# Optimization experiments

Hardware: AMD Instinct MI355X
Metric: run time of the kernel (lower is better)

## Reference

```python
import jax, jax.numpy as jnp
import numpy as np


def setup_inputs() -> dict:
    key = jax.random.key(0)
    ks = jax.random.split(key, 6)
    B, N, S, D, A = 32, 12, 512, 256, 96
    return {
        "value": jax.random.normal(ks[0], (B, N, S, D), dtype=jnp.float32),
        "emb": jax.random.normal(ks[1], (N, S, A), dtype=jnp.float32),
        "Wqk": jax.random.normal(ks[2], (A, D), dtype=jnp.float32) * (A ** -0.5),
        "bqk": jax.random.normal(ks[3], (D,), dtype=jnp.float32) * 0.02,
        "Wv": jax.random.normal(ks[4], (D, D), dtype=jnp.float32) * (D ** -0.5),
        "bv": jax.random.normal(ks[5], (D,), dtype=jnp.float32) * 0.02,
    }


def reference(value, emb, Wqk, bqk, Wv, bv):
    # qk: [n, s, d] -- query and key share the same projection FC_Q_K
    qk = emb @ Wqk + bqk
    v = value @ Wv + bv                      # [b, n, s, d]
    q = jax.nn.softmax(qk, axis=-1)          # softmax over d (last dim of query)
    k = jax.nn.softmax(qk.swapaxes(-1, -2), axis=-1)  # [n, d, s], softmax over s
    # key @ value: [n, d, s] x [b, n, s, e] -> [b, n, d, e] (broadcast over b)
    kv = jnp.einsum('nds,bnse->bnde', k, v)
    # query @ kv: [n, s, d] x [b, n, d, e] -> [b, n, s, e]
    out = jnp.einsum('nsd,bnde->bnse', q, kv)
    return out
```

## Files before the change

### kernel.cpp

```cpp
#include <hip/hip_runtime.h>
#include <hip/hip_bf16.h>

#define B_ 32
#define N_ 12
#define S_ 512
#define D_ 256
#define A_ 96

typedef __attribute__((ext_vector_type(8))) short short8;
typedef __attribute__((ext_vector_type(4))) float float4v;

static __device__ __forceinline__ ushort f2bf(float f) {
  union { float f; unsigned u; } a;
  a.f = f;
  return (ushort)((a.u + 0x7FFFu + ((a.u >> 16) & 1u)) >> 16);
}

__global__ __launch_bounds__(256) void k_qk_softmax_q(
    const float* __restrict__ emb, const float* __restrict__ Wqk,
    const float* __restrict__ bqk, float* __restrict__ qk,
    ushort* __restrict__ qb) {
  int ns = blockIdx.x;
  int d = threadIdx.x;
  __shared__ float se[A_];
  __shared__ float red[8];
  if (d < A_) se[d] = emb[ns * A_ + d];
  __syncthreads();
  float acc = bqk[d];
#pragma unroll
  for (int a = 0; a < A_; ++a) acc = fmaf(se[a], Wqk[a * D_ + d], acc);
  qk[ns * D_ + d] = acc;
  float m = acc;
  for (int off = 32; off; off >>= 1) m = fmaxf(m, __shfl_xor(m, off));
  if ((d & 63) == 0) red[d >> 6] = m;
  __syncthreads();
  m = fmaxf(fmaxf(red[0], red[1]), fmaxf(red[2], red[3]));
  float e = __expf(acc - m);
  float sum = e;
  for (int off = 32; off; off >>= 1) sum += __shfl_xor(sum, off);
  if ((d & 63) == 0) red[4 + (d >> 6)] = sum;
  __syncthreads();
  sum = red[4] + red[5] + red[6] + red[7];
  qb[ns * D_ + d] = f2bf(e / sum);
}

__global__ __launch_bounds__(256) void k_softmax_kT(
    const float* __restrict__ qk, ushort* __restrict__ kTb) {
  int d = blockIdx.x;
  int n = blockIdx.y;
  int s = threadIdx.x;
  __shared__ float red[8];
  float v0 = qk[(n * S_ + s) * D_ + d];
  float v1 = qk[(n * S_ + s + 256) * D_ + d];
  float m = fmaxf(v0, v1);
  for (int off = 32; off; off >>= 1) m = fmaxf(m, __shfl_xor(m, off));
  if ((s & 63) == 0) red[s >> 6] = m;
  __syncthreads();
  m = fmaxf(fmaxf(red[0], red[1]), fmaxf(red[2], red[3]));
  float e0 = __expf(v0 - m), e1 = __expf(v1 - m);
  float sum = e0 + e1;
  for (int off = 32; off; off >>= 1) sum += __shfl_xor(sum, off);
  if ((s & 63) == 0) red[4 + (s >> 6)] = sum;
  __syncthreads();
  sum = red[4] + red[5] + red[6] + red[7];
  float inv = 1.0f / sum;
  kTb[(n * D_ + d) * S_ + s] = f2bf(e0 * inv);
  kTb[(n * D_ + d) * S_ + s + 256] = f2bf(e1 * inv);
}

__global__ __launch_bounds__(256) void k_wvt(const float* __restrict__ Wv,
                                             ushort* __restrict__ WvT) {
  int c = blockIdx.x, e = threadIdx.x;
  WvT[c * D_ + e] = f2bf(Wv[e * D_ + c]);
}

__global__ __launch_bounds__(256) void k_kv0(
    const ushort* __restrict__ kTb, const float* __restrict__ value,
    ushort* __restrict__ kv0) {
  const int eb = blockIdx.x * 64;
  const int bz = blockIdx.y;
  const int n = bz % N_;
  const int tid = threadIdx.x;
  const int l = tid & 63, w = tid >> 6;
  const int lane16 = l & 15, quad = l >> 4;

  __shared__ ushort ldsV[64 * 72];
  __shared__ ushort ldsK[256 * 72];

  float4v acc[4][4];
#pragma unroll
  for (int i = 0; i < 4; ++i)
#pragma unroll
    for (int j = 0; j < 4; ++j) acc[i][j] = (float4v)0.0f;

  const ushort* kTbase = kTb + (size_t)n * D_ * S_;
  const float* vbase = value + (size_t)bz * S_ * D_ + eb;

  for (int sc = 0; sc < S_; sc += 64) {
    __syncthreads();
#pragma unroll
    for (int it = 0; it < 8; ++it) {
      int id = it * 256 + tid;
      int rd = id >> 3, cc = (id & 7) * 8;
      *(uint4*)(&ldsK[rd * 72 + cc]) =
          *(const uint4*)(kTbase + rd * S_ + sc + cc);
    }
#pragma unroll
    for (int it = 0; it < 8; ++it) {
      int id = it * 256 + tid;
      int e = id & 63, sp = id >> 6;
      float f0 = vbase[(sc + 2 * sp) * D_ + e];
      float f1 = vbase[(sc + 2 * sp + 1) * D_ + e];
      ushort2 p;
      p.x = f2bf(f0);
      p.y = f2bf(f1);
      *(ushort2*)(&ldsV[e * 72 + 2 * sp]) = p;
    }
    __syncthreads();
#pragma unroll
    for (int kc = 0; kc < 64; kc += 32) {
      int ko = kc + quad * 8;
      short8 a[4], b[4];
#pragma unroll
      for (int i = 0; i < 4; ++i)
        a[i] = *(const short8*)(&ldsV[(i * 16 + lane16) * 72 + ko]);
#pragma unroll
      for (int j = 0; j < 4; ++j)
        b[j] = *(const short8*)(&ldsK[(w * 64 + j * 16 + lane16) * 72 + ko]);
#pragma unroll
      for (int i = 0; i < 4; ++i)
#pragma unroll
        for (int j = 0; j < 4; ++j)
          acc[i][j] = __builtin_amdgcn_mfma_f32_16x16x32_bf16(a[i], b[j],
                                                              acc[i][j], 0, 0, 0);
    }
  }
  ushort* obase = kv0 + (size_t)bz * D_ * D_;
#pragma unroll
  for (int i = 0; i < 4; ++i) {
#pragma unroll
    for (int j = 0; j < 4; ++j) {
      int d = w * 64 + j * 16 + lane16;
      int e0 = eb + i * 16 + quad * 4;
      ushort4 p;
      p.x = f2bf(acc[i][j][0]);
      p.y = f2bf(acc[i][j][1]);
      p.z = f2bf(acc[i][j][2]);
      p.w = f2bf(acc[i][j][3]);
      *(ushort4*)(obase + d * D_ + e0) = p;
    }
  }
}

__global__ __launch_bounds__(256) void k_kvw_inplace(
    ushort* kv0, const ushort* __restrict__ WvT,
    const float* __restrict__ bv) {
  const int h = blockIdx.x;
  const int bz = blockIdx.y;
  const int tid = threadIdx.x;
  const int l = tid & 63, w = tid >> 6;
  const int lane16 = l & 15, quad = l >> 4;

  __shared__ ushort ldsA[128 * 72];
  __shared__ ushort ldsB[256 * 72];

  float4v acc[2][4][4];
#pragma unroll
  for (int m = 0; m < 2; ++m)
#pragma unroll
    for (int i = 0; i < 4; ++i)
#pragma unroll
      for (int j = 0; j < 4; ++j) acc[m][i][j] = (float4v)0.0f;

  ushort* base = kv0 + (size_t)bz * (D_ * D_) + h * (128 * D_);

  for (int ec = 0; ec < D_; ec += 64) {
    __syncthreads();
#pragma unroll
    for (int it = 0; it < 4; ++it) {
      int id = it * 256 + tid;
      int rd = id >> 3, cc = (id & 7) * 8;
      *(uint4*)(&ldsA[rd * 72 + cc]) =
          *(const uint4*)(base + rd * D_ + ec + cc);
    }
#pragma unroll
    for (int it = 0; it < 8; ++it) {
      int id = it * 256 + tid;
      int rd = id >> 3, cc = (id & 7) * 8;
      *(uint4*)(&ldsB[rd * 72 + cc]) =
          *(const uint4*)(WvT + rd * D_ + ec + cc);
    }
    __syncthreads();
#pragma unroll
    for (int kc = 0; kc < 64; kc += 32) {
      int ko = kc + quad * 8;
      short8 a[2][4], b[4];
#pragma unroll
      for (int m = 0; m < 2; ++m)
#pragma unroll
        for (int i = 0; i < 4; ++i)
          a[m][i] =
              *(const short8*)(&ldsA[(m * 64 + i * 16 + lane16) * 72 + ko]);
#pragma unroll
      for (int j = 0; j < 4; ++j)
        b[j] = *(const short8*)(&ldsB[(w * 64 + j * 16 + lane16) * 72 + ko]);
#pragma unroll
      for (int m = 0; m < 2; ++m)
#pragma unroll
        for (int i = 0; i < 4; ++i)
#pragma unroll
          for (int j = 0; j < 4; ++j)
            acc[m][i][j] = __builtin_amdgcn_mfma_f32_16x16x32_bf16(
                a[m][i], b[j], acc[m][i][j], 0, 0, 0);
    }
  }
#pragma unroll
  for (int m = 0; m < 2; ++m) {
#pragma unroll
    for (int i = 0; i < 4; ++i) {
#pragma unroll
      for (int j = 0; j < 4; ++j) {
        int c = w * 64 + j * 16 + lane16;
        int d0 = m * 64 + i * 16 + quad * 4;
        float bvc = bv[c];
        ushort4 p;
        p.x = f2bf(acc[m][i][j][0] + bvc);
        p.y = f2bf(acc[m][i][j][1] + bvc);
        p.z = f2bf(acc[m][i][j][2] + bvc);
        p.w = f2bf(acc[m][i][j][3] + bvc);
        *(ushort4*)(base + c * 128 + d0) = p;
      }
    }
  }
}

__global__ __launch_bounds__(256) void k_out(
    const ushort* __restrict__ qb, const ushort* __restrict__ kvw,
    float* __restrict__ out) {
  const int bx = blockIdx.x;
  const int by = blockIdx.y;
  const int bz = blockIdx.z;
  const int n = bz % N_;
  const int tid = threadIdx.x;
  const int l = tid & 63, w = tid >> 6;
  const int wm = w & 1, wn = w >> 1;
  const int lane16 = l & 15, quad = l >> 4;

  __shared__ ushort ldsA[128 * 72];
  __shared__ ushort ldsB[128 * 72];

  float4v acc[4][4];
#pragma unroll
  for (int i = 0; i < 4; ++i)
#pragma unroll
    for (int j = 0; j < 4; ++j) acc[i][j] = (float4v)0.0f;

  const ushort* abase = qb + (size_t)n * S_ * D_ + bx * 128 * D_;
  const ushort* bbase = kvw + (size_t)bz * D_ * D_;

  for (int dc = 0; dc < D_; dc += 64) {
    __syncthreads();
#pragma unroll
    for (int it = 0; it < 4; ++it) {
      int id = it * 256 + tid;
      int rd = id >> 3, cc = (id & 7) * 8;
      *(uint4*)(&ldsA[rd * 72 + cc]) =
          *(const uint4*)(abase + rd * D_ + dc + cc);
    }
#pragma unroll
    for (int it = 0; it < 4; ++it) {
      int id = it * 256 + tid;
      int rd = id >> 3, cc = (id & 7) * 8;
      *(uint4*)(&ldsB[rd * 72 + cc]) =
          *(const uint4*)(bbase + (dc >> 7) * 32768 + (by * 128 + rd) * 128 +
                          (dc & 127) + cc);
    }
    __syncthreads();
#pragma unroll
    for (int kc = 0; kc < 64; kc += 32) {
      int ko = kc + quad * 8;
      short8 a[4], b[4];
#pragma unroll
      for (int i = 0; i < 4; ++i)
        a[i] = *(const short8*)(&ldsA[(wm * 64 + i * 16 + lane16) * 72 + ko]);
#pragma unroll
      for (int j = 0; j < 4; ++j)
        b[j] = *(const short8*)(&ldsB[(wn * 64 + j * 16 + lane16) * 72 + ko]);
#pragma unroll
      for (int i = 0; i < 4; ++i)
#pragma unroll
        for (int j = 0; j < 4; ++j)
          acc[i][j] = __builtin_amdgcn_mfma_f32_16x16x32_bf16(a[i], b[j],
                                                              acc[i][j], 0, 0, 0);
    }
  }
  float* obase = out + (size_t)bz * S_ * D_;
#pragma unroll
  for (int i = 0; i < 4; ++i) {
#pragma unroll
    for (int j = 0; j < 4; ++j) {
      int s0 = bx * 128 + wm * 64 + i * 16 + quad * 4;
      int c = by * 128 + wn * 64 + j * 16 + lane16;
#pragma unroll
      for (int r = 0; r < 4; ++r)
        obase[(s0 + r) * D_ + c] = acc[i][j][r];
    }
  }
}

extern "C" void kernel_launch(void* const* d_in, const int* in_sizes, int n_in,
                              void* d_out, int out_size, void* d_ws,
                              size_t ws_size, hipStream_t stream) {
  const float* value = (const float*)d_in[0];
  const float* emb   = (const float*)d_in[1];
  const float* Wqk   = (const float*)d_in[2];
  const float* bqk   = (const float*)d_in[3];
  const float* Wv    = (const float*)d_in[4];
  const float* bv    = (const float*)d_in[5];
  float* out = (float*)d_out;

  char* ws = (char*)d_ws;
  float*  qk  = (float*)ws;
  ushort* qb  = (ushort*)(ws + 6291456);
  ushort* kTb = (ushort*)(ws + 9437184);
  ushort* kv0 = (ushort*)(ws + 12582912);
  ushort* WvT = (ushort*)(ws + 62914560);

  k_qk_softmax_q<<<dim3(N_ * S_), 256, 0, stream>>>(emb, Wqk, bqk, qk, qb);
  k_softmax_kT<<<dim3(D_, N_), 256, 0, stream>>>(qk, kTb);
  k_wvt<<<dim3(D_), 256, 0, stream>>>(Wv, WvT);
  k_kv0<<<dim3(4, B_ * N_), 256, 0, stream>>>(kTb, value, kv0);
  k_kvw_inplace<<<dim3(2, B_ * N_), 256, 0, stream>>>(kv0, WvT, bv);
  k_out<<<dim3(4, 2, B_ * N_), 256, 0, stream>>>(qb, kv0, out);
}
```

Baseline: 472.4 us.

## Batch rows in qk projection, tile kT softmax via LDS, vectorize V staging, split kvw

The qk projection kernel now handles 8 rows per block so each Wqk load is reused eight times. The key softmax stages a 16-column tile transposed through shared memory, which replaces strided single-float reads. V staging packs 4 rows per ushort4 LDS store. The in-place kv×Wv kernel now uses 64-row blocks with twice as many blocks, and k_out's addressing is adjusted to the new layout. The aim is less global traffic and more parallelism, at the cost of larger shared-memory tiles and more registers per thread.

```diff
diff --git a/kernel.cpp b/kernel.cpp
--- a/kernel.cpp
+++ b/kernel.cpp
@@ -20,52 +20,109 @@
     const float* __restrict__ emb, const float* __restrict__ Wqk,
     const float* __restrict__ bqk, float* __restrict__ qk,
     ushort* __restrict__ qb) {
-  int ns = blockIdx.x;
-  int d = threadIdx.x;
-  __shared__ float se[A_];
-  __shared__ float red[8];
-  if (d < A_) se[d] = emb[ns * A_ + d];
+  const int blk = blockIdx.x;
+  const int tid = threadIdx.x;
+  const int d = tid;
+  const int wv = tid >> 6, lane = tid & 63;
+  __shared__ float seT[A_][8];
+  __shared__ float redm[8][4], reds[8][4];
+  const float* ebase = emb + (size_t)blk * 8 * A_;
+  for (int k = tid; k < 8 * A_; k += 256) {
+    int r = k / A_, a = k - r * A_;
+    seT[a][r] = ebase[k];
+  }
   __syncthreads();
-  float acc = bqk[d];
-#pragma unroll
-  for (int a = 0; a < A_; ++a) acc = fmaf(se[a], Wqk[a * D_ + d], acc);
-  qk[ns * D_ + d] = acc;
-  float m = acc;
-  for (int off = 32; off; off >>= 1) m = fmaxf(m, __shfl_xor(m, off));
-  if ((d & 63) == 0) red[d >> 6] = m;
+  float bq = bqk[d];
+  float acc[8];
+#pragma unroll
+  for (int r = 0; r < 8; ++r) acc[r] = bq;
+#pragma unroll 8
+  for (int a = 0; a < A_; ++a) {
+    float w = Wqk[a * D_ + d];
+    float4 lo = *(const float4*)(&seT[a][0]);
+    float4 hi = *(const float4*)(&seT[a][4]);
+    acc[0] = fmaf(lo.x, w, acc[0]);
+    acc[1] = fmaf(lo.y, w, acc[1]);
+    acc[2] = fmaf(lo.z, w, acc[2]);
+    acc[3] = fmaf(lo.w, w, acc[3]);
+    acc[4] = fmaf(hi.x, w, acc[4]);
+    acc[5] = fmaf(hi.y, w, acc[5]);
+    acc[6] = fmaf(hi.z, w, acc[6]);
+    acc[7] = fmaf(hi.w, w, acc[7]);
+  }
+  const size_t obase = (size_t)blk * 8 * D_ + d;
+#pragma unroll
+  for (int r = 0; r < 8; ++r) qk[obase + r * D_] = acc[r];
+  float m[8];
+#pragma unroll
+  for (int r = 0; r < 8; ++r) {
+    m[r] = acc[r];
+    for (int off = 32; off; off >>= 1) m[r] = fmaxf(m[r], __shfl_xor(m[r], off));
+  }
+  if (lane == 0) {
+#pragma unroll
+    for (int r = 0; r < 8; ++r) redm[r][wv] = m[r];
+  }
   __syncthreads();
-  m = fmaxf(fmaxf(red[0], red[1]), fmaxf(red[2], red[3]));
-  float e = __expf(acc - m);
-  float sum = e;
-  for (int off = 32; off; off >>= 1) sum += __shfl_xor(sum, off);
-  if ((d & 63) == 0) red[4 + (d >> 6)] = sum;
+  float e[8], s[8];
+#pragma unroll
+  for (int r = 0; r < 8; ++r) {
+    float mm = fmaxf(fmaxf(redm[r][0], redm[r][1]),
+                     fmaxf(redm[r][2], redm[r][3]));
+    e[r] = __expf(acc[r] - mm);
+    s[r] = e[r];
+    for (int off = 32; off; off >>= 1) s[r] += __shfl_xor(s[r], off);
+  }
+  if (lane == 0) {
+#pragma unroll
+    for (int r = 0; r < 8; ++r) reds[r][wv] = s[r];
+  }
   __syncthreads();
-  sum = red[4] + red[5] + red[6] + red[7];
-  qb[ns * D_ + d] = f2bf(e / sum);
+#pragma unroll
+  for (int r = 0; r < 8; ++r) {
+    float sum = reds[r][0] + reds[r][1] + reds[r][2] + reds[r][3];
+    qb[obase + r * D_] = f2bf(e[r] / sum);
+  }
 }
 
 __global__ __launch_bounds__(256) void k_softmax_kT(
     const float* __restrict__ qk, ushort* __restrict__ kTb) {
-  int d = blockIdx.x;
-  int n = blockIdx.y;
-  int s = threadIdx.x;
-  __shared__ float red[8];
-  float v0 = qk[(n * S_ + s) * D_ + d];
-  float v1 = qk[(n * S_ + s + 256) * D_ + d];
-  float m = fmaxf(v0, v1);
-  for (int off = 32; off; off >>= 1) m = fmaxf(m, __shfl_xor(m, off));
-  if ((s & 63) == 0) red[s >> 6] = m;
+  const int dc = blockIdx.x * 16;
+  const int n = blockIdx.y;
+  const int tid = threadIdx.x;
+  __shared__ float t[16][514];
+  const float* base = qk + (size_t)n * S_ * D_ + dc;
+#pragma unroll
+  for (int it = 0; it < 8; ++it) {
+    int id = it * 256 + tid;
+    int d4 = id & 3, s = id >> 2;
+    float4 v = *(const float4*)(base + (size_t)s * D_ + 4 * d4);
+    t[4 * d4 + 0][s] = v.x;
+    t[4 * d4 + 1][s] = v.y;
+    t[4 * d4 + 2][s] = v.z;
+    t[4 * d4 + 3][s] = v.w;
+  }
   __syncthreads();
-  m = fmaxf(fmaxf(red[0], red[1]), fmaxf(red[2], red[3]));
-  float e0 = __expf(v0 - m), e1 = __expf(v1 - m);
-  float sum = e0 + e1;
-  for (int off = 32; off; off >>= 1) sum += __shfl_xor(sum, off);
-  if ((s & 63) == 0) red[4 + (s >> 6)] = sum;
-  __syncthreads();
-  sum = red[4] + red[5] + red[6] + red[7];
+  const int d = tid >> 4, sg = tid & 15;
+  float vv[32];
+  float m = -1e30f;
+#pragma unroll
+  for (int k = 0; k < 32; ++k) {
+    vv[k] = t[d][sg + 16 * k];
+    m = fmaxf(m, vv[k]);
+  }
+  for (int off = 1; off < 16; off <<= 1) m = fmaxf(m, __shfl_xor(m, off));
+  float sum = 0.0f;
+#pragma unroll
+  for (int k = 0; k < 32; ++k) {
+    vv[k] = __expf(vv[k] - m);
+    sum += vv[k];
+  }
+  for (int off = 1; off < 16; off <<= 1) sum += __shfl_xor(sum, off);
   float inv = 1.0f / sum;
-  kTb[(n * D_ + d) * S_ + s] = f2bf(e0 * inv);
-  kTb[(n * D_ + d) * S_ + s + 256] = f2bf(e1 * inv);
+  const size_t ob = ((size_t)n * D_ + dc + d) * S_;
+#pragma unroll
+  for (int k = 0; k < 32; ++k) kTb[ob + sg + 16 * k] = f2bf(vv[k] * inv);
 }
 
 __global__ __launch_bounds__(256) void k_wvt(const float* __restrict__ Wv,
@@ -106,15 +163,19 @@
           *(const uint4*)(kTbase + rd * S_ + sc + cc);
     }
 #pragma unroll
-    for (int it = 0; it < 8; ++it) {
-      int id = it * 256 + tid;
-      int e = id & 63, sp = id >> 6;
-      float f0 = vbase[(sc + 2 * sp) * D_ + e];
-      float f1 = vbase[(sc + 2 * sp + 1) * D_ + e];
-      ushort2 p;
+    for (int it = 0; it < 4; ++it) {
+      int id = it * 256 + tid;
+      int e = id & 63, sq = id >> 6;
+      float f0 = vbase[(sc + 4 * sq + 0) * D_ + e];
+      float f1 = vbase[(sc + 4 * sq + 1) * D_ + e];
+      float f2 = vbase[(sc + 4 * sq + 2) * D_ + e];
+      float f3 = vbase[(sc + 4 * sq + 3) * D_ + e];
+      ushort4 p;
       p.x = f2bf(f0);
       p.y = f2bf(f1);
-      *(ushort2*)(&ldsV[e * 72 + 2 * sp]) = p;
+      p.z = f2bf(f2);
+      p.w = f2bf(f3);
+      *(ushort4*)(&ldsV[e * 72 + 4 * sq]) = p;
     }
     __syncthreads();
 #pragma unroll
@@ -155,29 +216,27 @@
 __global__ __launch_bounds__(256) void k_kvw_inplace(
     ushort* kv0, const ushort* __restrict__ WvT,
     const float* __restrict__ bv) {
-  const int h = blockIdx.x;
+  const int qd = blockIdx.x;
   const int bz = blockIdx.y;
   const int tid = threadIdx.x;
   const int l = tid & 63, w = tid >> 6;
   const int lane16 = l & 15, quad = l >> 4;
 
-  __shared__ ushort ldsA[128 * 72];
+  __shared__ ushort ldsA[64 * 72];
   __shared__ ushort ldsB[256 * 72];
 
-  float4v acc[2][4][4];
-#pragma unroll
-  for (int m = 0; m < 2; ++m)
-#pragma unroll
-    for (int i = 0; i < 4; ++i)
-#pragma unroll
-      for (int j = 0; j < 4; ++j) acc[m][i][j] = (float4v)0.0f;
-
-  ushort* base = kv0 + (size_t)bz * (D_ * D_) + h * (128 * D_);
+  float4v acc[4][4];
+#pragma unroll
+  for (int i = 0; i < 4; ++i)
+#pragma unroll
+    for (int j = 0; j < 4; ++j) acc[i][j] = (float4v)0.0f;
+
+  ushort* base = kv0 + (size_t)bz * (D_ * D_) + qd * (64 * D_);
 
   for (int ec = 0; ec < D_; ec += 64) {
     __syncthreads();
 #pragma unroll
-    for (int it = 0; it < 4; ++it) {
+    for (int it = 0; it < 2; ++it) {
       int id = it * 256 + tid;
       int rd = id >> 3, cc = (id & 7) * 8;
       *(uint4*)(&ldsA[rd * 72 + cc]) =
@@ -194,42 +253,34 @@
 #pragma unroll
     for (int kc = 0; kc < 64; kc += 32) {
       int ko = kc + quad * 8;
-      short8 a[2][4], b[4];
-#pragma unroll
-      for (int m = 0; m < 2; ++m)
-#pragma unroll
-        for (int i = 0; i < 4; ++i)
-          a[m][i] =
-              *(const short8*)(&ldsA[(m * 64 + i * 16 + lane16) * 72 + ko]);
+      short8 a[4], b[4];
+#pragma unroll
+      for (int i = 0; i < 4; ++i)
+        a[i] = *(const short8*)(&ldsA[(i * 16 + lane16) * 72 + ko]);
 #pragma unroll
       for (int j = 0; j < 4; ++j)
         b[j] = *(const short8*)(&ldsB[(w * 64 + j * 16 + lane16) * 72 + ko]);
 #pragma unroll
-      for (int m = 0; m < 2; ++m)
-#pragma unroll
-        for (int i = 0; i < 4; ++i)
-#pragma unroll
-          for (int j = 0; j < 4; ++j)
-            acc[m][i][j] = __builtin_amdgcn_mfma_f32_16x16x32_bf16(
-                a[m][i], b[j], acc[m][i][j], 0, 0, 0);
-    }
-  }
-#pragma unroll
-  for (int m = 0; m < 2; ++m) {
-#pragma unroll
-    for (int i = 0; i < 4; ++i) {
-#pragma unroll
-      for (int j = 0; j < 4; ++j) {
-        int c = w * 64 + j * 16 + lane16;
-        int d0 = m * 64 + i * 16 + quad * 4;
-        float bvc = bv[c];
-        ushort4 p;
-        p.x = f2bf(acc[m][i][j][0] + bvc);
-        p.y = f2bf(acc[m][i][j][1] + bvc);
-        p.z = f2bf(acc[m][i][j][2] + bvc);
-        p.w = f2bf(acc[m][i][j][3] + bvc);
-        *(ushort4*)(base + c * 128 + d0) = p;
-      }
+      for (int i = 0; i < 4; ++i)
+#pragma unroll
+        for (int j = 0; j < 4; ++j)
+          acc[i][j] = __builtin_amdgcn_mfma_f32_16x16x32_bf16(a[i], b[j],
+                                                              acc[i][j], 0, 0, 0);
+    }
+  }
+#pragma unroll
+  for (int i = 0; i < 4; ++i) {
+#pragma unroll
+    for (int j = 0; j < 4; ++j) {
+      int c = w * 64 + j * 16 + lane16;
+      int d0 = i * 16 + quad * 4;
+      float bvc = bv[c];
+      ushort4 p;
+      p.x = f2bf(acc[i][j][0] + bvc);
+      p.y = f2bf(acc[i][j][1] + bvc);
+      p.z = f2bf(acc[i][j][2] + bvc);
+      p.w = f2bf(acc[i][j][3] + bvc);
+      *(ushort4*)(base + c * 64 + d0) = p;
     }
   }
 }
@@ -272,8 +323,8 @@
       int id = it * 256 + tid;
       int rd = id >> 3, cc = (id & 7) * 8;
       *(uint4*)(&ldsB[rd * 72 + cc]) =
-          *(const uint4*)(bbase + (dc >> 7) * 32768 + (by * 128 + rd) * 128 +
-                          (dc & 127) + cc);
+          *(const uint4*)(bbase + (dc >> 6) * 16384 + (by * 128 + rd) * 64 +
+                          cc);
     }
     __syncthreads();
 #pragma unroll
@@ -326,10 +377,10 @@
   ushort* kv0 = (ushort*)(ws + 12582912);
   ushort* WvT = (ushort*)(ws + 62914560);
 
-  k_qk_softmax_q<<<dim3(N_ * S_), 256, 0, stream>>>(emb, Wqk, bqk, qk, qb);
-  k_softmax_kT<<<dim3(D_, N_), 256, 0, stream>>>(qk, kTb);
+  k_qk_softmax_q<<<dim3(N_ * S_ / 8), 256, 0, stream>>>(emb, Wqk, bqk, qk, qb);
+  k_softmax_kT<<<dim3(16, N_), 256, 0, stream>>>(qk, kTb);
   k_wvt<<<dim3(D_), 256, 0, stream>>>(Wv, WvT);
   k_kv0<<<dim3(4, B_ * N_), 256, 0, stream>>>(kTb, value, kv0);
-  k_kvw_inplace<<<dim3(2, B_ * N_), 256, 0, stream>>>(kv0, WvT, bv);
+  k_kvw_inplace<<<dim3(4, B_ * N_), 256, 0, stream>>>(kv0, WvT, bv);
   k_out<<<dim3(4, 2, B_ * N_), 256, 0, stream>>>(qb, kv0, out);
 }
```

After: 445.6 us. -5.7%, faster.
